# Performance work log

Measured on AMD Instinct MI355X. Metric: run time of the kernel, lower is better.

## Reference

```python
import jax, jax.numpy as jnp
import numpy as np

B, S, HID = 4, 2048, 768
H, DBLK, HD = 12, 256, 64  # heads, block_dim = HID//3, head_dim


def setup_inputs() -> dict:
    key = jax.random.key(0)
    ks = jax.random.split(key, 7)
    scale = 0.02
    return {
        "inputs": jax.random.normal(ks[0], (B, S, HID), jnp.float32),
        "Wq": jax.random.normal(ks[1], (H, DBLK, HD), jnp.float32) * scale,
        "bq": jax.random.normal(ks[2], (H, HD), jnp.float32) * scale,
        "Wk": jax.random.normal(ks[3], (H, DBLK, HD), jnp.float32) * scale,
        "bk": jax.random.normal(ks[4], (H, HD), jnp.float32) * scale,
        "Wv": jax.random.normal(ks[5], (H, DBLK, HD), jnp.float32) * scale,
        "bv": jax.random.normal(ks[6], (H, HD), jnp.float32) * scale,
    }


def reference(inputs, Wq, bq, Wk, bk, Wv, bv):
    b, s, hid = inputs.shape
    h, dblk, hd = Wq.shape
    hpm = h // 3  # heads per modality
    # split hidden into 3 modality blocks: [B, S, 3, DBLK]
    xm = inputs.reshape(b, s, 3, dblk)

    def proj(W, bias):
        # block-diagonal GEMM: each modality's x projected by its hpm heads
        y = jnp.einsum('bsmd,mhde->bmhse', xm, W.reshape(3, hpm, dblk, hd))
        y = y + bias.reshape(3, hpm, 1, hd)
        return y.reshape(b, h, s, hd)

    Q = proj(Wq, bq)
    K = proj(Wk, bk)
    V = proj(Wv, bv)

    scores = jnp.einsum('bhse,bhte->bhst', Q, K) / jnp.sqrt(jnp.float32(hd))
    probs = jax.nn.softmax(scores, axis=-1)  # dropout p=0 -> identity
    ctx = jnp.einsum('bhst,bhte->bhse', probs, V)
    # concat heads along feature dim: [B, S, H*HD]
    return ctx.transpose(0, 2, 1, 3).reshape(b, s, h * hd)
```

## Files before the change

kernel.cpp:

```cpp
#include <hip/hip_runtime.h>
#include <hip/hip_bf16.h>

#define B_    4
#define S_    2048
#define HID_  768
#define H_    12
#define DBLK_ 256
#define HD_   64
#define BH_   (B_ * H_)
#define QSZ_  (B_ * H_ * S_ * HD_)
#define WTSZ_ (3 * H_ * HD_ * DBLK_)

typedef _Float16 f16x4 __attribute__((ext_vector_type(4)));
typedef _Float16 f16x8 __attribute__((ext_vector_type(8)));
typedef float    f32x4 __attribute__((ext_vector_type(4)));

#if __has_builtin(__builtin_amdgcn_exp2f)
#define EXP2(x) __builtin_amdgcn_exp2f(x)
#else
#define EXP2(x) exp2f(x)
#endif

typedef const void __attribute__((address_space(1)))* gptr_t;
typedef       void __attribute__((address_space(3)))* sptr_t;

__global__ __launch_bounds__(256) void wconv(
    const float* __restrict__ Wq, const float* __restrict__ Wk,
    const float* __restrict__ Wv, _Float16* __restrict__ whf)
{
    const int idx  = blockIdx.x * 256 + threadIdx.x;
    const int j    = idx & 7;
    const int lane = (idx >> 3) & 63;
    const int et   = (idx >> 9) & 1;
    const int kk   = (idx >> 10) & 7;
    const int eh   = (idx >> 13) & 1;
    const int ph   = idx >> 14;
    const int h    = ph % H_;
    const int p    = ph / H_;
    const int e = eh * 32 + et * 16 + (lane & 15);
    const int k = kk * 32 + (lane >> 4) * 8 + j;
    const float* W = (p == 0) ? Wq : (p == 1) ? Wk : Wv;
    whf[idx] = (_Float16)W[((size_t)h * DBLK_ + k) * HD_ + e];
}

__global__ __launch_bounds__(256, 3) void qkv_proj(
    const float* __restrict__ x, const _Float16* __restrict__ whf,
    const float* __restrict__ bq, const float* __restrict__ bk,
    const float* __restrict__ bv,
    _Float16* __restrict__ qo, _Float16* __restrict__ khf,
    _Float16* __restrict__ vtf)
{
    const int i   = blockIdx.x;
    const int g   = i >> 7;
    const int sc  = i & 127;
    const int m   = g >> 1;
    const int s0g = sc * 64;

    const int tid  = threadIdx.x;
    const int lane = tid & 63;
    const int w    = tid >> 6;
    const int ln   = lane & 15;
    const int qd   = lane >> 4;
    const int h    = 2 * g + (w >> 1);
    const int eh   = w & 1;

    __shared__ _Float16 xs[64 * 256];

    {
        const int rr   = tid >> 6;
        const int c4   = tid & 63;
        const int g16  = c4 >> 1;
        const int half = c4 & 1;
        #pragma unroll
        for (int pass = 0; pass < 16; pass++) {
            const int r = pass * 4 + rr;
            const float4 v = *(const float4*)(
                x + (size_t)(s0g + r) * HID_ + m * DBLK_ + c4 * 4);
            f16x4 hv;
            hv[0] = (_Float16)v.x; hv[1] = (_Float16)v.y;
            hv[2] = (_Float16)v.z; hv[3] = (_Float16)v.w;
            *(f16x4*)(xs + r * 256 + ((g16 ^ (r & 7)) * 8) + half * 4) = hv;
        }
    }
    __syncthreads();

    f32x4 acc[3][2][4];
    #pragma unroll
    for (int p = 0; p < 3; p++)
        #pragma unroll
        for (int et = 0; et < 2; et++)
            #pragma unroll
            for (int st = 0; st < 4; st++)
                acc[p][et][st] = (f32x4){0.f, 0.f, 0.f, 0.f};

    const _Float16* wb = whf + (size_t)((h * 2 + eh) * 16) * 512 + lane * 8;

    for (int kk = 0; kk < 8; kk++) {
        f16x8 a[4];
        #pragma unroll
        for (int st = 0; st < 4; st++)
            a[st] = *(const f16x8*)(
                xs + (st * 16 + ln) * 256 + (((kk * 4 + qd) ^ (ln & 7)) * 8));
        #pragma unroll
        for (int p = 0; p < 3; p++)
            #pragma unroll
            for (int et = 0; et < 2; et++) {
                const f16x8 bb = *(const f16x8*)(
                    wb + (size_t)p * 196608 + (kk * 2 + et) * 512);
                #pragma unroll
                for (int st = 0; st < 4; st++)
                    acc[p][et][st] = __builtin_amdgcn_mfma_f32_16x16x32_f16(
                        a[st], bb, acc[p][et][st], 0, 0, 0);
            }
    }

    const float QS = 0.18033688011112042f;
    const int b    = s0g >> 11;
    const int s0   = s0g & 2047;
    const int bhh  = b * H_ + h;
    const int tile = s0 >> 6;
    const size_t tb = (size_t)(bhh * 32 + tile) * 4096;

    #pragma unroll
    for (int et = 0; et < 2; et++) {
        const int d  = eh * 32 + et * 16 + ln;
        const int dc = d >> 3, d7 = d & 7;
        const float biasq = bq[h * HD_ + d];
        const float biask = bk[h * HD_ + d];
        const float biasv = bv[h * HD_ + d];
        const int dn = eh * 2 + et;
        #pragma unroll
        for (int st = 0; st < 4; st++) {
            #pragma unroll
            for (int r = 0; r < 4; r++) {
                const int sl = st * 16 + qd * 4 + r;
                qo[((size_t)bhh * S_ + s0 + sl) * HD_ + d] =
                    (_Float16)((acc[0][et][st][r] + biasq) * QS);
                khf[tb + sl * 64 + ((dc ^ (sl & 7)) * 8) + d7] =
                    (_Float16)(acc[1][et][st][r] + biask);
            }
            f16x4 vv;
            #pragma unroll
            for (int r = 0; r < 4; r++) vv[r] = (_Float16)(acc[2][et][st][r] + biasv);
            const int chunk = (qd * 2 + (st >> 1)) ^ (ln & 7);
            *(f16x4*)(vtf + tb + dn * 1024 + ln * 64 + chunk * 8 + (st & 1) * 4) = vv;
        }
    }
}

__global__ __launch_bounds__(256, 3) void attn(
    const _Float16* __restrict__ qh, const _Float16* __restrict__ khf,
    const _Float16* __restrict__ vtf, float* __restrict__ out)
{
    const int i    = blockIdx.x;
    const int slot = i >> 3;
    const int bh   = (i & 7) * 6 + (slot % 6);
    const int qt   = slot / 6;
    const int h = bh % H_, b = bh / H_;
    const int q0 = qt * 128;

    const int tid  = threadIdx.x;
    const int lane = tid & 63;
    const int w    = tid >> 6;
    const int ln   = lane & 15;
    const int qd   = lane >> 4;

    __shared__ __align__(16) char lds[2][16384];

    f16x8 qf[2][2];
    #pragma unroll
    for (int st = 0; st < 2; st++) {
        const _Float16* qb = qh + ((size_t)bh * S_ + q0 + w * 32 + st * 16 + ln) * HD_;
        qf[st][0] = *(const f16x8*)(qb + qd * 8);
        qf[st][1] = *(const f16x8*)(qb + 32 + qd * 8);
    }

    f32x4 o[2][4];
    float lr[2] = {0.f, 0.f};
    #pragma unroll
    for (int st = 0; st < 2; st++)
        #pragma unroll
        for (int dn = 0; dn < 4; dn++) o[st][dn] = (f32x4){0.f, 0.f, 0.f, 0.f};

    const char* kbase = (const char*)(khf + (size_t)bh * 32 * 4096);
    const char* vbase = (const char*)(vtf + (size_t)bh * 32 * 4096);
    const int   seg   = w * 1024 + lane * 16;
    const int   wseg  = w * 1024;

    auto dma = [&](int it, int buf) {
        const char* ks = kbase + (size_t)it * 8192;
        const char* vs = vbase + (size_t)it * 8192;
        char* lk = &lds[buf][0];
        char* lv = &lds[buf][8192];
        #pragma unroll
        for (int q = 0; q < 2; q++) {
            __builtin_amdgcn_global_load_lds(
                (gptr_t)(ks + q * 4096 + seg), (sptr_t)(lk + q * 4096 + wseg), 16, 0, 0);
            __builtin_amdgcn_global_load_lds(
                (gptr_t)(vs + q * 4096 + seg), (sptr_t)(lv + q * 4096 + wseg), 16, 0, 0);
        }
    };

    dma(0, 0);

    for (int it = 0; it < 32; it++) {
        const int buf = it & 1;
        __syncthreads();
        if (it + 1 < 32) dma(it + 1, buf ^ 1);

        const char* lk = &lds[buf][0];
        const char* lv = &lds[buf][8192];

        f16x8 kf[4][2];
        #pragma unroll
        for (int mt = 0; mt < 4; mt++) {
            kf[mt][0] = *(const f16x8*)(lk + (16 * mt + ln) * 128 + ((qd       ^ (ln & 7)) * 16));
            kf[mt][1] = *(const f16x8*)(lk + (16 * mt + ln) * 128 + (((4 + qd) ^ (ln & 7)) * 16));
        }
        f16x8 v8[4][2];
        #pragma unroll
        for (int dn = 0; dn < 4; dn++)
            #pragma unroll
            for (int hf = 0; hf < 2; hf++)
                v8[dn][hf] = *(const f16x8*)(
                    lv + dn * 2048 + ln * 128 + (((qd * 2 + hf) ^ (ln & 7)) * 16));

        #pragma unroll
        for (int st = 0; st < 2; st++) {
            f16x4 a[4];
            #pragma unroll
            for (int mt = 0; mt < 4; mt++) {
                f32x4 s = (f32x4){0.f, 0.f, 0.f, 0.f};
                s = __builtin_amdgcn_mfma_f32_16x16x32_f16(kf[mt][0], qf[st][0], s, 0, 0, 0);
                s = __builtin_amdgcn_mfma_f32_16x16x32_f16(kf[mt][1], qf[st][1], s, 0, 0, 0);
                const float p0 = EXP2(s[0]), p1 = EXP2(s[1]);
                const float p2 = EXP2(s[2]), p3 = EXP2(s[3]);
                lr[st] += (p0 + p1) + (p2 + p3);
                f16x4 av;
                av[0] = (_Float16)p0; av[1] = (_Float16)p1;
                av[2] = (_Float16)p2; av[3] = (_Float16)p3;
                a[mt] = av;
            }
            #pragma unroll
            for (int dn = 0; dn < 4; dn++)
                #pragma unroll
                for (int c = 0; c < 4; c++) {
                    const f16x8 vv8 = v8[dn][c >> 1];
                    const f16x4 vv = (c & 1)
                        ? __builtin_shufflevector(vv8, vv8, 4, 5, 6, 7)
                        : __builtin_shufflevector(vv8, vv8, 0, 1, 2, 3);
                    o[st][dn] = __builtin_amdgcn_mfma_f32_16x16x16f16(a[c], vv, o[st][dn], 0, 0, 0);
                }
        }
    }

    #pragma unroll
    for (int st = 0; st < 2; st++) {
        float l = lr[st];
        l += __shfl_xor(l, 16);
        l += __shfl_xor(l, 32);
        float inv[4];
        #pragma unroll
        for (int r = 0; r < 4; r++)
            inv[r] = 1.f / __shfl(l, qd * 4 + r, 16);
        #pragma unroll
        for (int dn = 0; dn < 4; dn++) {
            float* op = out + ((size_t)b * S_ + q0 + w * 32 + st * 16 + qd * 4) * HID_
                      + (size_t)h * HD_ + dn * 16 + ln;
            #pragma unroll
            for (int r = 0; r < 4; r++)
                op[(size_t)r * HID_] = o[st][dn][r] * inv[r];
        }
    }
}

extern "C" void kernel_launch(void* const* d_in, const int* in_sizes, int n_in,
                              void* d_out, int out_size, void* d_ws, size_t ws_size,
                              hipStream_t stream) {
    const float* x  = (const float*)d_in[0];
    const float* Wq = (const float*)d_in[1];
    const float* bq = (const float*)d_in[2];
    const float* Wk = (const float*)d_in[3];
    const float* bk = (const float*)d_in[4];
    const float* Wv = (const float*)d_in[5];
    const float* bv = (const float*)d_in[6];
    float* out = (float*)d_out;

    _Float16* q  = (_Float16*)d_ws;
    _Float16* k  = q + QSZ_;
    _Float16* vt = k + QSZ_;
    const size_t need = ((size_t)3 * QSZ_ + WTSZ_) * sizeof(_Float16);
    _Float16* wh = (ws_size >= need) ? (vt + QSZ_)
                                     : (_Float16*)d_out;

    wconv<<<WTSZ_ / 256, 256, 0, stream>>>(Wq, Wk, Wv, wh);
    qkv_proj<<<768, 256, 0, stream>>>(x, wh, bq, bk, bv, q, k, vt);
    attn<<<768, 256, 0, stream>>>(q, k, vt, out);
}
```

Measured before the change: 178.2 us.

## Use 16x16x32 MFMA for PV and row sums, restage QK tiles via LDS

```diff
diff --git a/kernel.cpp b/kernel.cpp
--- a/kernel.cpp
+++ b/kernel.cpp
@@ -119,32 +119,53 @@
     const int s0   = s0g & 2047;
     const int bhh  = b * H_ + h;
     const int tile = s0 >> 6;
-    const size_t tb = (size_t)(bhh * 32 + tile) * 4096;
-
-    #pragma unroll
-    for (int et = 0; et < 2; et++) {
-        const int d  = eh * 32 + et * 16 + ln;
-        const int dc = d >> 3, d7 = d & 7;
-        const float biasq = bq[h * HD_ + d];
-        const float biask = bk[h * HD_ + d];
-        const float biasv = bv[h * HD_ + d];
-        const int dn = eh * 2 + et;
-        #pragma unroll
-        for (int st = 0; st < 4; st++) {
-            #pragma unroll
-            for (int r = 0; r < 4; r++) {
-                const int sl = st * 16 + qd * 4 + r;
-                qo[((size_t)bhh * S_ + s0 + sl) * HD_ + d] =
-                    (_Float16)((acc[0][et][st][r] + biasq) * QS);
-                khf[tb + sl * 64 + ((dc ^ (sl & 7)) * 8) + d7] =
-                    (_Float16)(acc[1][et][st][r] + biask);
+    const int ht   = w >> 1;
+
+    __syncthreads();
+    {
+        _Float16* qtile = xs + ht * 4096;
+        _Float16* ktile = xs + 8192 + ht * 4096;
+        const size_t tbv = (size_t)(bhh * 32 + tile) * 4096;
+        #pragma unroll
+        for (int et = 0; et < 2; et++) {
+            const int d  = eh * 32 + et * 16 + ln;
+            const int dc = d >> 3, d7 = d & 7;
+            const float biasq = bq[h * HD_ + d];
+            const float biask = bk[h * HD_ + d];
+            const float biasv = bv[h * HD_ + d];
+            #pragma unroll
+            for (int st = 0; st < 4; st++) {
+                f16x4 vv;
+                #pragma unroll
+                for (int r = 0; r < 4; r++) vv[r] = (_Float16)(acc[2][et][st][r] + biasv);
+                const int vc = st * 2 + (qd >> 1);
+                *(f16x4*)(vtf + tbv + d * 64 + ((vc ^ d7) * 8) + (qd & 1) * 4) = vv;
+                #pragma unroll
+                for (int r = 0; r < 4; r++) {
+                    const int sl  = st * 16 + qd * 4 + r;
+                    const int rho = (st >> 1) * 32 + (qd & 1) * 16
+                                  + ((st & 1) * 2 + (qd >> 1)) * 4 + r;
+                    qtile[sl  * 64 + ((dc ^ (sl  & 7)) * 8) + d7] =
+                        (_Float16)((acc[0][et][st][r] + biasq) * QS);
+                    ktile[rho * 64 + ((dc ^ (rho & 7)) * 8) + d7] =
+                        (_Float16)(acc[1][et][st][r] + biask);
+                }
             }
-            f16x4 vv;
-            #pragma unroll
-            for (int r = 0; r < 4; r++) vv[r] = (_Float16)(acc[2][et][st][r] + biasv);
-            const int chunk = (qd * 2 + (st >> 1)) ^ (ln & 7);
-            *(f16x4*)(vtf + tb + dn * 1024 + ln * 64 + chunk * 8 + (st & 1) * 4) = vv;
-        }
+        }
+    }
+    __syncthreads();
+    #pragma unroll
+    for (int it = 0; it < 4; it++) {
+        const int idx  = it * 256 + tid;
+        const int ht2  = idx >> 9;
+        const int rest = idx & 511;
+        const int row  = rest >> 3;
+        const int c    = rest & 7;
+        const int bhh2 = b * H_ + 2 * g + ht2;
+        const f16x8 qv = *(const f16x8*)(xs + ht2 * 4096 + row * 64 + ((c ^ (row & 7)) * 8));
+        *(f16x8*)(qo + ((size_t)bhh2 * S_ + s0 + row) * HD_ + c * 8) = qv;
+        const f16x8 kv8 = *(const f16x8*)(xs + 8192 + ht2 * 4096 + row * 64 + c * 8);
+        *(f16x8*)(khf + (size_t)(bhh2 * 32 + tile) * 4096 + row * 64 + c * 8) = kv8;
     }
 }
 
@@ -175,12 +196,18 @@
         qf[st][1] = *(const f16x8*)(qb + 32 + qd * 8);
     }
 
+    f16x8 ones;
+    #pragma unroll
+    for (int j = 0; j < 8; j++) ones[j] = (_Float16)1.f;
+
     f32x4 o[2][4];
-    float lr[2] = {0.f, 0.f};
-    #pragma unroll
-    for (int st = 0; st < 2; st++)
+    f32x4 lacc[2];
+    #pragma unroll
+    for (int st = 0; st < 2; st++) {
+        lacc[st] = (f32x4){0.f, 0.f, 0.f, 0.f};
         #pragma unroll
         for (int dn = 0; dn < 4; dn++) o[st][dn] = (f32x4){0.f, 0.f, 0.f, 0.f};
+    }
 
     const char* kbase = (const char*)(khf + (size_t)bh * 32 * 4096);
     const char* vbase = (const char*)(vtf + (size_t)bh * 32 * 4096);
@@ -217,52 +244,48 @@
             kf[mt][0] = *(const f16x8*)(lk + (16 * mt + ln) * 128 + ((qd       ^ (ln & 7)) * 16));
             kf[mt][1] = *(const f16x8*)(lk + (16 * mt + ln) * 128 + (((4 + qd) ^ (ln & 7)) * 16));
         }
-        f16x8 v8[4][2];
+        f16x8 vf[4][2];
         #pragma unroll
         for (int dn = 0; dn < 4; dn++)
             #pragma unroll
-            for (int hf = 0; hf < 2; hf++)
-                v8[dn][hf] = *(const f16x8*)(
-                    lv + dn * 2048 + ln * 128 + (((qd * 2 + hf) ^ (ln & 7)) * 16));
+            for (int p = 0; p < 2; p++)
+                vf[dn][p] = *(const f16x8*)(
+                    lv + (dn * 16 + ln) * 128 + (((p * 4 + qd) ^ (ln & 7)) * 16));
 
         #pragma unroll
         for (int st = 0; st < 2; st++) {
-            f16x4 a[4];
+            f32x4 s[4];
             #pragma unroll
             for (int mt = 0; mt < 4; mt++) {
-                f32x4 s = (f32x4){0.f, 0.f, 0.f, 0.f};
-                s = __builtin_amdgcn_mfma_f32_16x16x32_f16(kf[mt][0], qf[st][0], s, 0, 0, 0);
-                s = __builtin_amdgcn_mfma_f32_16x16x32_f16(kf[mt][1], qf[st][1], s, 0, 0, 0);
-                const float p0 = EXP2(s[0]), p1 = EXP2(s[1]);
-                const float p2 = EXP2(s[2]), p3 = EXP2(s[3]);
-                lr[st] += (p0 + p1) + (p2 + p3);
-                f16x4 av;
-                av[0] = (_Float16)p0; av[1] = (_Float16)p1;
-                av[2] = (_Float16)p2; av[3] = (_Float16)p3;
-                a[mt] = av;
+                s[mt] = (f32x4){0.f, 0.f, 0.f, 0.f};
+                s[mt] = __builtin_amdgcn_mfma_f32_16x16x32_f16(kf[mt][0], qf[st][0], s[mt], 0, 0, 0);
+                s[mt] = __builtin_amdgcn_mfma_f32_16x16x32_f16(kf[mt][1], qf[st][1], s[mt], 0, 0, 0);
             }
             #pragma unroll
-            for (int dn = 0; dn < 4; dn++)
+            for (int p = 0; p < 2; p++) {
+                f16x8 a8;
+                a8[0] = (_Float16)EXP2(s[2 * p][0]);
+                a8[1] = (_Float16)EXP2(s[2 * p][1]);
+                a8[2] = (_Float16)EXP2(s[2 * p][2]);
+                a8[3] = (_Float16)EXP2(s[2 * p][3]);
+                a8[4] = (_Float16)EXP2(s[2 * p + 1][0]);
+                a8[5] = (_Float16)EXP2(s[2 * p + 1][1]);
+                a8[6] = (_Float16)EXP2(s[2 * p + 1][2]);
+                a8[7] = (_Float16)EXP2(s[2 * p + 1][3]);
+                lacc[st] = __builtin_amdgcn_mfma_f32_16x16x32_f16(a8, ones, lacc[st], 0, 0, 0);
                 #pragma unroll
-                for (int c = 0; c < 4; c++) {
-                    const f16x8 vv8 = v8[dn][c >> 1];
-                    const f16x4 vv = (c & 1)
-                        ? __builtin_shufflevector(vv8, vv8, 4, 5, 6, 7)
-                        : __builtin_shufflevector(vv8, vv8, 0, 1, 2, 3);
-                    o[st][dn] = __builtin_amdgcn_mfma_f32_16x16x16f16(a[c], vv, o[st][dn], 0, 0, 0);
-                }
+                for (int dn = 0; dn < 4; dn++)
+                    o[st][dn] = __builtin_amdgcn_mfma_f32_16x16x32_f16(
+                        a8, vf[dn][p], o[st][dn], 0, 0, 0);
+            }
         }
     }
 
     #pragma unroll
     for (int st = 0; st < 2; st++) {
-        float l = lr[st];
-        l += __shfl_xor(l, 16);
-        l += __shfl_xor(l, 32);
         float inv[4];
         #pragma unroll
-        for (int r = 0; r < 4; r++)
-            inv[r] = 1.f / __shfl(l, qd * 4 + r, 16);
+        for (int r = 0; r < 4; r++) inv[r] = 1.f / lacc[st][r];
         #pragma unroll
         for (int dn = 0; dn < 4; dn++) {
             float* op = out + ((size_t)b * S_ + q0 + w * 32 + st * 16 + qd * 4) * HID_
```

After: 170.0 us. 1.05x faster.
